# Optimization experiments

Hardware: AMD Instinct MI355X
Metric: run time of the kernel (lower is better)

## Reference

```python
import jax, jax.numpy as jnp
import numpy as np

N_NODES = 100000
K = 5
C = 16
E = 3200000  # nonzeros per shift power


def setup_inputs() -> dict:
    key = jax.random.key(0)
    k1, k2, k3, k4, k5 = jax.random.split(key, 5)
    X = jax.random.normal(k1, (N_NODES, C), dtype=jnp.float32)
    rows = jax.random.randint(k2, (K, E), 0, N_NODES, dtype=jnp.int32)
    cols = jax.random.randint(k3, (K, E), 0, N_NODES, dtype=jnp.int32)
    vals = jax.random.normal(k4, (K, E), dtype=jnp.float32)
    h = jax.random.normal(k5, (C, K), dtype=jnp.float32)  # per-channel filter taps
    return {"X": X, "rows": rows, "cols": cols, "vals": vals, "h": h}


def reference(X, rows, cols, vals, h):
    # Original math: y = sum_c sum_k h[c,k] * (S_k @ X[:, c])
    #              = sum_k S_k @ (X @ h[:, k])
    N = X.shape[0]
    Kp, Ep = rows.shape
    Z = X @ h  # [N, K] combined per-tap signals
    # gather Z at source nodes for each tap: Zg[k, e] = Z[cols[k, e], k]
    Zg = Z[cols, jnp.arange(Kp, dtype=cols.dtype)[:, None]]  # [K, E]
    contrib = vals * Zg  # [K, E]
    y = jax.ops.segment_sum(contrib.reshape(-1), rows.reshape(-1), num_segments=N)
    return y  # [N]
```

## Files before the change

### kernel.cpp

```cpp
#include <hip/hip_runtime.h>
#include <hip/hip_fp16.h>

#define N_NODES 100000
#define KK 5
#define CC 16
#define EE 3200000
#define NXCC 8

#define NB 16
#define ROWS_PB 6250
#define WCAP 384
#define WPAD 385
#define BPB 64
#define CHUNK 5120
#define NCHUNK 3125
#define BLK_PER_K 625
#define SGRID 256
#define STHREADS 1024

typedef unsigned int uint2v __attribute__((ext_vector_type(2)));

__device__ __forceinline__ int xcc_id() {
    int x;
    asm volatile("s_getreg_b32 %0, hwreg(HW_REG_XCC_ID)" : "=s"(x));
    return x & (NXCC - 1);
}

__global__ void compute_z_kernel(const float* __restrict__ X,
                                 const float* __restrict__ h,
                                 float* __restrict__ Zt,
                                 __half* __restrict__ Zh) {
    int n = blockIdx.x * blockDim.x + threadIdx.x;
    if (n >= N_NODES) return;
    const float4* Xr = (const float4*)(X + (size_t)n * CC);
    float4 x0 = Xr[0], x1 = Xr[1], x2 = Xr[2], x3 = Xr[3];
    float xv[CC] = {x0.x, x0.y, x0.z, x0.w, x1.x, x1.y, x1.z, x1.w,
                    x2.x, x2.y, x2.z, x2.w, x3.x, x3.y, x3.z, x3.w};
#pragma unroll
    for (int k = 0; k < KK; ++k) {
        float acc = 0.0f;
#pragma unroll
        for (int c = 0; c < CC; ++c) acc += xv[c] * h[c * KK + k];
        Zt[k * N_NODES + n] = acc;
        Zh[k * N_NODES + n] = __float2half_rn(acc);
    }
}

template<int SN>
__global__ __launch_bounds__(STHREADS, 1)
void scatter_lds_kernel(const int* __restrict__ rows,
                        const int* __restrict__ cols,
                        const float* __restrict__ vals,
                        const __half* __restrict__ Zh,
                        unsigned int* __restrict__ binned,
                        int* __restrict__ counts,
                        float* __restrict__ spill) {
    extern __shared__ char dynlds[];
    __half*       zsl = (__half*)dynlds;
    unsigned int* buf = (unsigned int*)(dynlds + (size_t)SN * 2);
    __shared__ int lcnt[NB];
    int tid = threadIdx.x;
    int bid = blockIdx.x;
    int w0 = (int)(((long long)NCHUNK * bid) / SGRID);
    int w1 = (int)(((long long)NCHUNK * (bid + 1)) / SGRID);

    int klast = -1;
    for (int w = w0; w < w1; ++w) {
        int k = w / BLK_PER_K;
        const __half* Zk_h = Zh + (size_t)k * N_NODES;
        if (SN > 0 && k != klast) {
            __syncthreads();
            const float4* zsrc = (const float4*)Zk_h;
            float4*       zdst = (float4*)dynlds;
#pragma unroll
            for (int i = 0; i < SN / 8192; ++i)
                zdst[tid + i * 1024] = zsrc[tid + i * 1024];
            klast = k;
            __syncthreads();
        }
        if (tid < NB) lcnt[tid] = 0;
        __syncthreads();

        int cbase = w * CHUNK;
        int e0 = cbase + tid * 4;
        int e4 = cbase + 4096 + tid;
        int4   r0 = *(const int4*)(rows + e0);
        int4   c0 = *(const int4*)(cols + e0);
        float4 v0 = *(const float4*)(vals + e0);
        int    r1 = rows[e4];
        int    c1 = cols[e4];
        float  v1 = vals[e4];

        int   cix[5] = {c0.x, c0.y, c0.z, c0.w, c1};
        int   rr[5]  = {r0.x, r0.y, r0.z, r0.w, r1};
        float vv[5]  = {v0.x, v0.y, v0.z, v0.w, v1};

        float z[5];
#pragma unroll
        for (int i = 0; i < 5; ++i) {
            unsigned c = (unsigned)cix[i];
            __half hz;
            if (SN > 0 && c < (unsigned)SN) hz = zsl[c];
            else                            hz = Zk_h[c];
            z[i] = __half2float(hz);
        }

        int pos[5];
#pragma unroll
        for (int i = 0; i < 5; ++i) {
            int b = rr[i] / ROWS_PB;
            pos[i] = atomicAdd(&lcnt[b], 1);
        }

#pragma unroll
        for (int i = 0; i < 5; ++i) {
            int b = rr[i] / ROWS_PB;
            float cb = vv[i] * z[i];
            int p = pos[i];
            if (p < WCAP) {
                unsigned int packed =
                    ((unsigned)(rr[i] - b * ROWS_PB) << 16) |
                    (unsigned)__half_as_ushort(__float2half_rn(cb));
                buf[b * WPAD + p] = packed;
            } else {
                unsafeAtomicAdd(&spill[rr[i]], cb);
            }
        }
        __syncthreads();

        unsigned int* wbase = binned + (size_t)w * WCAP;
#pragma unroll 1
        for (int b = 0; b < NB; ++b) {
            int cnt = min(lcnt[b], WCAP);
            if (tid < cnt)
                wbase[(size_t)b * ((size_t)NCHUNK * WCAP) + tid] = buf[b * WPAD + tid];
        }
        if (tid < NB) counts[w * NB + tid] = min(lcnt[tid], WCAP);
        __syncthreads();
    }
}

__global__ __launch_bounds__(512, 2)
void accum_kernel(const unsigned int* __restrict__ binned,
                  const int* __restrict__ counts,
                  float* __restrict__ partials) {
    __shared__ float acc[ROWS_PB];
    __shared__ int cnts[56];
    int b = blockIdx.x / BPB;
    int s = blockIdx.x % BPB;
    int tid = threadIdx.x;
    int wlo = (NCHUNK * s) / BPB;
    int whi = (NCHUNK * (s + 1)) / BPB;
    for (int i = tid; i < ROWS_PB; i += 512) acc[i] = 0.0f;
    if (tid < whi - wlo) cnts[tid] = counts[(wlo + tid) * NB + b];
    __syncthreads();

    const unsigned int* bbase = binned + (size_t)b * ((size_t)NCHUNK * WCAP);
    int t    = tid & 255;
    int half = tid >> 8;
    for (int w0 = wlo; w0 < whi; w0 += 16) {
        uint2v e[8];
        int ok0[8], ok1[8];
#pragma unroll
        for (int j = 0; j < 8; ++j) {
            int w = w0 + 2 * j + half;
            int cnt = (w < whi) ? cnts[w - wlo] : 0;
            ok0[j] = 2 * t < cnt;
            ok1[j] = 2 * t + 1 < cnt;
            const uint2v* src = (const uint2v*)(bbase + (size_t)w * WCAP);
            uint2v ez = {0u, 0u};
            e[j] = ok0[j] ? src[t] : ez;
        }
#pragma unroll
        for (int j = 0; j < 8; ++j) {
            if (ok0[j])
                atomicAdd(&acc[e[j][0] >> 16],
                          __half2float(__ushort_as_half((unsigned short)(e[j][0] & 0xFFFFu))));
            if (ok1[j])
                atomicAdd(&acc[e[j][1] >> 16],
                          __half2float(__ushort_as_half((unsigned short)(e[j][1] & 0xFFFFu))));
        }
    }
    __syncthreads();
    float* dst = partials + (size_t)blockIdx.x * ROWS_PB;
    for (int i = tid; i < ROWS_PB; i += 512) dst[i] = acc[i];
}

__global__ void reduce_kernel(const float* __restrict__ partials,
                              const float* __restrict__ spill,
                              float* __restrict__ y) {
    int n = blockIdx.x * blockDim.x + threadIdx.x;
    if (n >= N_NODES) return;
    int b = n / ROWS_PB, loc = n - b * ROWS_PB;
    const float* p = partials + (size_t)(b * BPB) * ROWS_PB + loc;
    float acc = spill[n];
#pragma unroll 8
    for (int s = 0; s < BPB; ++s) acc += p[(size_t)s * ROWS_PB];
    y[n] = acc;
}

__global__ void edge_kernel_atomic(const int* __restrict__ rows,
                                   const int* __restrict__ cols,
                                   const float* __restrict__ vals,
                                   const float* __restrict__ Zt,
                                   float* __restrict__ yrep) {
    int t = blockIdx.x * blockDim.x + threadIdx.x;
    int base = t * 4;
    if (base >= KK * EE) return;
    int k = base / EE;
    const float* Zk = Zt + (size_t)k * N_NODES;
    float* y = yrep + (size_t)xcc_id() * N_NODES;
    int4 r = *(const int4*)(rows + base);
    int4 c = *(const int4*)(cols + base);
    float4 v = *(const float4*)(vals + base);
    unsafeAtomicAdd(&y[r.x], v.x * Zk[c.x]);
    unsafeAtomicAdd(&y[r.y], v.y * Zk[c.y]);
    unsafeAtomicAdd(&y[r.z], v.z * Zk[c.z]);
    unsafeAtomicAdd(&y[r.w], v.w * Zk[c.w]);
}

__global__ void reduce8_kernel(const float* __restrict__ yrep, float* __restrict__ y) {
    int n = blockIdx.x * blockDim.x + threadIdx.x;
    if (n >= N_NODES) return;
    float acc = 0.0f;
#pragma unroll
    for (int r = 0; r < NXCC; ++r) acc += yrep[(size_t)r * N_NODES + n];
    y[n] = acc;
}

extern "C" void kernel_launch(void* const* d_in, const int* in_sizes, int n_in,
                              void* d_out, int out_size, void* d_ws, size_t ws_size,
                              hipStream_t stream) {
    const float* X    = (const float*)d_in[0];
    const int*   rows = (const int*)  d_in[1];
    const int*   cols = (const int*)  d_in[2];
    const float* vals = (const float*)d_in[3];
    const float* h    = (const float*)d_in[4];
    float* y = (float*)d_out;

    char* ws = (char*)d_ws;
    float*  Zt = (float*)ws;
    size_t zh_off      = 2000000;
    size_t counts_off  = 3000000;
    size_t spill_off   = 3200000;
    size_t binned_off  = 3600000;
    size_t binned_sz   = (size_t)NCHUNK * NB * WCAP * 4;
    size_t partial_off = binned_off + binned_sz;
    size_t partial_sz  = (size_t)NB * BPB * ROWS_PB * 4;
    size_t need = partial_off + partial_sz;
    __half* Zh = (__half*)(ws + zh_off);

    {
        int threads = 256;
        int blocks  = (N_NODES + threads - 1) / threads;
        compute_z_kernel<<<blocks, threads, 0, stream>>>(X, h, Zt, Zh);
    }

    if (ws_size >= need) {
        int*          counts   = (int*)(ws + counts_off);
        float*        spill    = (float*)(ws + spill_off);
        unsigned int* binned   = (unsigned int*)(ws + binned_off);
        float*        partials = (float*)(ws + partial_off);
        hipMemsetAsync(spill, 0, 400000, stream);

        static int g_sn = -1;
        const size_t stag = (size_t)NB * WPAD * 4;
        if (g_sn < 0) {
            g_sn = 0;
            int nb = 0;
            hipFuncSetAttribute((const void*)scatter_lds_kernel<65536>,
                                hipFuncAttributeMaxDynamicSharedMemorySize,
                                (int)(65536 * 2 + stag));
            if (hipOccupancyMaxActiveBlocksPerMultiprocessor(
                    &nb, scatter_lds_kernel<65536>, STHREADS, 65536 * 2 + stag) == hipSuccess
                && nb >= 1) g_sn = 65536;
            if (g_sn == 0) {
                nb = 0;
                hipFuncSetAttribute((const void*)scatter_lds_kernel<49152>,
                                    hipFuncAttributeMaxDynamicSharedMemorySize,
                                    (int)(49152 * 2 + stag));
                if (hipOccupancyMaxActiveBlocksPerMultiprocessor(
                        &nb, scatter_lds_kernel<49152>, STHREADS, 49152 * 2 + stag) == hipSuccess
                    && nb >= 1) g_sn = 49152;
            }
            if (g_sn == 0) {
                nb = 0;
                hipFuncSetAttribute((const void*)scatter_lds_kernel<32768>,
                                    hipFuncAttributeMaxDynamicSharedMemorySize,
                                    (int)(32768 * 2 + stag));
                if (hipOccupancyMaxActiveBlocksPerMultiprocessor(
                        &nb, scatter_lds_kernel<32768>, STHREADS, 32768 * 2 + stag) == hipSuccess
                    && nb >= 1) g_sn = 32768;
            }
        }
        size_t dyn = (size_t)g_sn * 2 + stag;
        switch (g_sn) {
        case 65536:
            scatter_lds_kernel<65536><<<SGRID, STHREADS, dyn, stream>>>(
                rows, cols, vals, Zh, binned, counts, spill);
            break;
        case 49152:
            scatter_lds_kernel<49152><<<SGRID, STHREADS, dyn, stream>>>(
                rows, cols, vals, Zh, binned, counts, spill);
            break;
        case 32768:
            scatter_lds_kernel<32768><<<SGRID, STHREADS, dyn, stream>>>(
                rows, cols, vals, Zh, binned, counts, spill);
            break;
        default:
            scatter_lds_kernel<0><<<SGRID, STHREADS, dyn, stream>>>(
                rows, cols, vals, Zh, binned, counts, spill);
            break;
        }

        accum_kernel<<<NB * BPB, 512, 0, stream>>>(binned, counts, partials);
        {
            int threads = 256;
            int blocks  = (N_NODES + threads - 1) / threads;
            reduce_kernel<<<blocks, threads, 0, stream>>>(partials, spill, y);
        }
    } else {
        float* yrep = (float*)(ws + spill_off);
        hipMemsetAsync(yrep, 0, (size_t)NXCC * N_NODES * sizeof(float), stream);
        {
            int threads = 256;
            int blocks = ((KK * EE) / 4 + threads - 1) / threads;
            edge_kernel_atomic<<<blocks, threads, 0, stream>>>(rows, cols, vals, Zt, yrep);
        }
        {
            int threads = 256;
            int blocks  = (N_NODES + threads - 1) / threads;
            reduce8_kernel<<<blocks, threads, 0, stream>>>(yrep, y);
        }
    }
}
```

Baseline: 329.3 us.

## Prefetch next chunk's edges and flatten binned write-out via prefix sums

The scatter kernel now issues the global loads for the next chunk's rows, cols and vals before processing the current chunk, so load latency overlaps with the LDS binning work. It also replaces the 16 serial per-bin write-out passes with one flattened loop over all binned entries, finding each entry's bin by binary search on a prefix-sum array built by thread 0. This uses more registers for the prefetched data and adds an extra barrier plus a serial prefix computation.

```diff
diff --git a/kernel.cpp b/kernel.cpp
--- a/kernel.cpp
+++ b/kernel.cpp
@@ -59,13 +59,35 @@
     __half*       zsl = (__half*)dynlds;
     unsigned int* buf = (unsigned int*)(dynlds + (size_t)SN * 2);
     __shared__ int lcnt[NB];
+    __shared__ int pfx[NB + 1];
     int tid = threadIdx.x;
     int bid = blockIdx.x;
     int w0 = (int)(((long long)NCHUNK * bid) / SGRID);
     int w1 = (int)(((long long)NCHUNK * (bid + 1)) / SGRID);
 
+    int4 rA, cA; float4 vA; int rsA, csA; float fsA;
+    {
+        int cbase = w0 * CHUNK;
+        rA  = *(const int4*)(rows + cbase + tid * 4);
+        cA  = *(const int4*)(cols + cbase + tid * 4);
+        vA  = *(const float4*)(vals + cbase + tid * 4);
+        int e4 = cbase + 4096 + tid;
+        rsA = rows[e4]; csA = cols[e4]; fsA = vals[e4];
+    }
+
     int klast = -1;
     for (int w = w0; w < w1; ++w) {
+        int4 rB = {}, cB = {}; float4 vB = {};
+        int rsB = 0, csB = 0; float fsB = 0.0f;
+        if (w + 1 < w1) {
+            int cb2 = (w + 1) * CHUNK;
+            rB  = *(const int4*)(rows + cb2 + tid * 4);
+            cB  = *(const int4*)(cols + cb2 + tid * 4);
+            vB  = *(const float4*)(vals + cb2 + tid * 4);
+            int e4 = cb2 + 4096 + tid;
+            rsB = rows[e4]; csB = cols[e4]; fsB = vals[e4];
+        }
+
         int k = w / BLK_PER_K;
         const __half* Zk_h = Zh + (size_t)k * N_NODES;
         if (SN > 0 && k != klast) {
@@ -81,19 +103,9 @@
         if (tid < NB) lcnt[tid] = 0;
         __syncthreads();
 
-        int cbase = w * CHUNK;
-        int e0 = cbase + tid * 4;
-        int e4 = cbase + 4096 + tid;
-        int4   r0 = *(const int4*)(rows + e0);
-        int4   c0 = *(const int4*)(cols + e0);
-        float4 v0 = *(const float4*)(vals + e0);
-        int    r1 = rows[e4];
-        int    c1 = cols[e4];
-        float  v1 = vals[e4];
-
-        int   cix[5] = {c0.x, c0.y, c0.z, c0.w, c1};
-        int   rr[5]  = {r0.x, r0.y, r0.z, r0.w, r1};
-        float vv[5]  = {v0.x, v0.y, v0.z, v0.w, v1};
+        int   cix[5] = {cA.x, cA.y, cA.z, cA.w, csA};
+        int   rr[5]  = {rA.x, rA.y, rA.z, rA.w, rsA};
+        float vv[5]  = {vA.x, vA.y, vA.z, vA.w, fsA};
 
         float z[5];
 #pragma unroll
@@ -128,15 +140,26 @@
         }
         __syncthreads();
 
+        if (tid == 0) {
+            int s = 0;
+#pragma unroll
+            for (int b = 0; b < NB; ++b) { pfx[b] = s; s += min(lcnt[b], WCAP); }
+            pfx[NB] = s;
+        }
+        __syncthreads();
+        int total = pfx[NB];
         unsigned int* wbase = binned + (size_t)w * WCAP;
-#pragma unroll 1
-        for (int b = 0; b < NB; ++b) {
-            int cnt = min(lcnt[b], WCAP);
-            if (tid < cnt)
-                wbase[(size_t)b * ((size_t)NCHUNK * WCAP) + tid] = buf[b * WPAD + tid];
+        for (int i = tid; i < total; i += STHREADS) {
+            int b = 0;
+#pragma unroll
+            for (int j = 8; j >= 1; j >>= 1)
+                if (pfx[b + j] <= i) b += j;
+            int p = i - pfx[b];
+            wbase[(size_t)b * ((size_t)NCHUNK * WCAP) + p] = buf[b * WPAD + p];
         }
         if (tid < NB) counts[w * NB + tid] = min(lcnt[tid], WCAP);
         __syncthreads();
+        rA = rB; cA = cB; vA = vB; rsA = rsB; csA = csB; fsA = fsB;
     }
 }
 
```

New measurement: 364.5 us. 10.7% more time.
